# Performance work log

Hardware: AMD Instinct MI355X
Metric: run time of the kernel (lower is better)

## Reference

```python
import jax, jax.numpy as jnp
import numpy as np
import math

B, C, H, W = 16, 512, 32, 32
NUM_HEADS = 8
EPS = 1e-5

def setup_inputs() -> dict:
    key = jax.random.key(0)
    ks = jax.random.split(key, 4)
    x = jax.random.normal(ks[0], (B, C, H, W), dtype=jnp.float32)
    emb = jax.random.normal(ks[1], (B, C), dtype=jnp.float32)
    w_qkv = jax.random.normal(ks[2], (3 * C, C), dtype=jnp.float32) * (1.0 / math.sqrt(C))
    b_qkv = jnp.zeros((3 * C,), dtype=jnp.float32)
    w_proj = jax.random.normal(ks[3], (C, C), dtype=jnp.float32) * (1.0 / math.sqrt(C))
    b_proj = jnp.zeros((C,), dtype=jnp.float32)
    return {"x": x, "emb": emb, "w_qkv": w_qkv, "b_qkv": b_qkv, "w_proj": w_proj, "b_proj": b_proj}


def reference(x, emb, w_qkv, b_qkv, w_proj, b_proj):
    b, c = x.shape[0], x.shape[1]
    spatial = x.shape[2:]
    xf = x.reshape(b, c, -1)                      # [b, c, T]
    # LayerNorm over channel dim (dim=1), no affine
    mu = jnp.mean(xf, axis=1, keepdims=True)
    var = jnp.var(xf, axis=1, keepdims=True)
    xn = (xf - mu) / jnp.sqrt(var + EPS)
    # 1x1 conv = channel GEMM: [3c,c] x [b,c,T] -> [b,3c,T]
    qkv = jnp.einsum('oc,bct->bot', w_qkv, xn) + b_qkv[None, :, None]
    T = qkv.shape[-1]
    qkv = qkv.reshape(b * NUM_HEADS, -1, T)       # [b*h, 3*hd, T]
    ch = qkv.shape[1] // 3
    q, k, v = jnp.split(qkv, 3, axis=1)
    scale = 1.0 / math.sqrt(math.sqrt(ch))
    w = jnp.einsum('bct,bcs->bts', q * scale, k * scale)  # [b*h, T, T]
    w = jax.nn.softmax(w.astype(jnp.float32), axis=-1).astype(qkv.dtype)
    h = jnp.einsum('bts,bcs->bct', w, v)          # [b*h, hd, T]
    h = h.reshape(b, -1, T)                        # [b, c, T]
    h = jnp.einsum('oc,bct->bot', w_proj, h) + b_proj[None, :, None]
    return (xf + h).reshape(b, c, *spatial)
```

## Files before the change

kernel.cpp:

```cpp
#include <hip/hip_runtime.h>


#define TSZ 1024
#define CCH 512
#define NBATCH 16

typedef __attribute__((ext_vector_type(8))) short short8;
typedef __attribute__((ext_vector_type(4))) float f32x4;

__device__ inline short f2bf(float f) {
  unsigned u = __builtin_bit_cast(unsigned, f);
  u += 0x7fff + ((u >> 16) & 1);
  return (short)(u >> 16);
}

__device__ inline void gl16(const void* g, void* l) {
  __builtin_amdgcn_global_load_lds((const __attribute__((address_space(1))) void*)g,
                                   (__attribute__((address_space(3))) void*)l,
                                   16, 0, 0);
}

__global__ __launch_bounds__(256) void k_cvt(const float* __restrict__ wq,
                                             const float* __restrict__ wp,
                                             short* __restrict__ wqb,
                                             short* __restrict__ wpb) {
  int i = blockIdx.x * 256 + threadIdx.x;
  const int nq = 1536 * 512;
  if (i < nq) wqb[i] = f2bf(wq[i]);
  int j = i - nq;
  if (j >= 0 && j < 512 * 512) wpb[j] = f2bf(wp[j]);
}

__global__ __launch_bounds__(256) void k_ln(const float* __restrict__ x,
                                            short* __restrict__ xnT) {
  const int b = blockIdx.x;
  const int t0 = blockIdx.y * 64;
  const int tid = threadIdx.x;
  const int tt = tid & 63, cg = tid >> 6;

  __shared__ float red[2][4][64];
  __shared__ float mu_s[64], rs_s[64];
  __shared__ float xt[64][65];

  const float* xb = x + (long)b * CCH * TSZ;

  float s = 0.f, s2 = 0.f;
  for (int c = cg * 128; c < cg * 128 + 128; ++c) {
    float v = xb[(long)c * TSZ + t0 + tt];
    s += v; s2 += v * v;
  }
  red[0][cg][tt] = s; red[1][cg][tt] = s2;
  __syncthreads();
  if (tid < 64) {
    float ss = red[0][0][tid] + red[0][1][tid] + red[0][2][tid] + red[0][3][tid];
    float qq = red[1][0][tid] + red[1][1][tid] + red[1][2][tid] + red[1][3][tid];
    float mu = ss * (1.f / 512.f);
    float var = qq * (1.f / 512.f) - mu * mu;
    mu_s[tid] = mu;
    rs_s[tid] = rsqrtf(var + 1e-5f);
  }
  __syncthreads();

  for (int c0 = 0; c0 < CCH; c0 += 64) {
    for (int i = tid; i < 64 * 64; i += 256) {
      int ci = i >> 6, t2 = i & 63;
      xt[ci][t2] = xb[(long)(c0 + ci) * TSZ + t0 + t2];
    }
    __syncthreads();
    for (int i = tid; i < 64 * 64; i += 256) {
      int cc = i & 63, t2 = i >> 6;
      float v = (xt[cc][t2] - mu_s[t2]) * rs_s[t2];
      xnT[((long)b * TSZ + t0 + t2) * CCH + c0 + cc] = f2bf(v);
    }
    __syncthreads();
  }
}

__device__ inline int qkmap(int n) {
  if (n < 512) return (n >> 6) * 192 + (n & 63);
  int j = n - 512;
  return (j >> 6) * 192 + 64 + (j & 63);
}
__device__ inline int vmap(int m) {
  return (m >> 6) * 192 + 128 + (m & 63);
}

template <int MODE>
__global__ __launch_bounds__(256) void k_gemm(const short* __restrict__ Ab,
                                              const short* __restrict__ Bb,
                                              void* __restrict__ outb,
                                              const float* __restrict__ bias,
                                              const float* __restrict__ resid) {
  const int b = blockIdx.z;
  const int m0 = blockIdx.x * 128, n0 = blockIdx.y * 128;
  const int tid = threadIdx.x;
  const int lane = tid & 63, wv = tid >> 6;
  const int wm = wv >> 1, wn = wv & 1;
  const int l15 = lane & 15, lg = lane >> 4;

  const short* A = Ab + (MODE == 0 ? (long)b * TSZ * CCH : 0);
  const short* Bm = Bb + (MODE == 0 ? 0 : (long)b * TSZ * CCH);

  __shared__ __attribute__((aligned(16))) short sA[128 * 32];
  __shared__ __attribute__((aligned(16))) short sB[128 * 32];

  f32x4 acc[4][4];
#pragma unroll
  for (int i = 0; i < 4; ++i)
#pragma unroll
    for (int j = 0; j < 4; ++j) acc[i][j] = (f32x4){0.f, 0.f, 0.f, 0.f};

  long a_src[2], b_src[2];
#pragma unroll
  for (int q = 0; q < 2; ++q) {
    int idx = wv * 128 + q * 64 + lane;
    int row = idx >> 2, kc = (idx & 3) * 8;
    int am = m0 + row;
    int ar = (MODE == 1) ? vmap(am) : am;
    a_src[q] = (long)ar * CCH + kc;
    int bn = n0 + row;
    int br = (MODE == 0) ? qkmap(bn) : bn;
    b_src[q] = (long)br * CCH + kc;
  }

  for (int k0 = 0; k0 < CCH; k0 += 32) {
#pragma unroll
    for (int q = 0; q < 2; ++q) {
      gl16(A + a_src[q] + k0, sA + (wv * 128 + q * 64) * 8);
      gl16(Bm + b_src[q] + k0, sB + (wv * 128 + q * 64) * 8);
    }
    __syncthreads();
    short8 af[4], bfr[4];
#pragma unroll
    for (int i = 0; i < 4; ++i)
      af[i] = *(const short8*)(sA + ((wm * 64 + i * 16 + l15) * 32 + lg * 8));
#pragma unroll
    for (int j = 0; j < 4; ++j)
      bfr[j] = *(const short8*)(sB + ((wn * 64 + j * 16 + l15) * 32 + lg * 8));
#pragma unroll
    for (int i = 0; i < 4; ++i)
#pragma unroll
      for (int j = 0; j < 4; ++j)
        acc[i][j] = __builtin_amdgcn_mfma_f32_16x16x32_bf16(af[i], bfr[j], acc[i][j], 0, 0, 0);
    __syncthreads();
  }

#pragma unroll
  for (int i = 0; i < 4; ++i)
#pragma unroll
    for (int j = 0; j < 4; ++j)
#pragma unroll
      for (int r = 0; r < 4; ++r) {
        int mi = m0 + wm * 64 + i * 16 + lg * 4 + r;
        int ni = n0 + wn * 64 + j * 16 + l15;
        float val = acc[i][j][r];
        long o = (long)mi * TSZ + ni;
        if (MODE == 0) {
          val += bias[qkmap(ni)];
          if (ni < 512) val *= 0.18033688011112042f;
          ((short*)outb)[(long)b * TSZ * TSZ + o] = f2bf(val);
        } else if (MODE == 1) {
          val += bias[vmap(mi)];
          ((short*)outb)[(long)b * CCH * TSZ + o] = f2bf(val);
        } else {
          val += bias[mi] + resid[(long)b * CCH * TSZ + o];
          ((float*)outb)[(long)b * CCH * TSZ + o] = val;
        }
      }
}

__global__ __launch_bounds__(256) void k_attn(const short* __restrict__ qk,
                                              const short* __restrict__ vbuf,
                                              short* __restrict__ hb) {
  const int bh = blockIdx.y;
  const int b = bh >> 3, h = bh & 7;
  const int t0 = blockIdx.x * 128;
  const int tid = threadIdx.x;
  const int lane = tid & 63, w = tid >> 6;
  const int l15 = lane & 15, lg = lane >> 4;

  __shared__ __attribute__((aligned(16))) short kt[64 * 64];
  __shared__ __attribute__((aligned(16))) short vt[64 * 64];
  __shared__ __attribute__((aligned(16))) short pt[4][32 * 64];

  const short* qkb = qk + (long)b * TSZ * 1024;
  const short* vb = vbuf + (long)b * CCH * TSZ;

  short8 aq[2][2];
  {
    const short* qb = qkb + (long)(t0 + w * 32) * 1024 + h * 64;
#pragma unroll
    for (int i = 0; i < 2; ++i)
#pragma unroll
      for (int kk = 0; kk < 2; ++kk)
        aq[i][kk] = *(const short8*)(qb + (long)(i * 16 + l15) * 1024 + kk * 32 + lg * 8);
  }

  f32x4 of[2][4];
  float lp[2][4];
#pragma unroll
  for (int i = 0; i < 2; ++i) {
#pragma unroll
    for (int nf = 0; nf < 4; ++nf) of[i][nf] = (f32x4){0.f, 0.f, 0.f, 0.f};
#pragma unroll
    for (int r = 0; r < 4; ++r) lp[i][r] = 0.f;
  }

  int srow[2], scoff[2];
#pragma unroll
  for (int q = 0; q < 2; ++q) {
    int idx = w * 128 + q * 64 + lane;
    int row = idx >> 3;
    int byo = ((idx & 7) * 16) ^ ((row & 7) << 4);
    srow[q] = row;
    scoff[q] = byo >> 1;
  }

  for (int s0 = 0; s0 < TSZ; s0 += 64) {
#pragma unroll
    for (int q = 0; q < 2; ++q) {
      gl16(qkb + (long)(s0 + srow[q]) * 1024 + 512 + h * 64 + scoff[q],
           kt + (w * 128 + q * 64) * 8);
      gl16(vb + ((long)(h * 64 + srow[q])) * TSZ + s0 + scoff[q],
           vt + (w * 128 + q * 64) * 8);
    }
    __syncthreads();

    f32x4 sf[2][4];
#pragma unroll
    for (int i = 0; i < 2; ++i)
#pragma unroll
      for (int nf = 0; nf < 4; ++nf) sf[i][nf] = (f32x4){0.f, 0.f, 0.f, 0.f};
#pragma unroll
    for (int kk = 0; kk < 2; ++kk)
#pragma unroll
      for (int nf = 0; nf < 4; ++nf) {
        int scol = nf * 16 + l15;
        int byo = ((scol * 64 + kk * 32 + lg * 8) * 2) ^ ((scol & 7) << 4);
        short8 bk = *(const short8*)((const char*)kt + byo);
#pragma unroll
        for (int i = 0; i < 2; ++i)
          sf[i][nf] = __builtin_amdgcn_mfma_f32_16x16x32_bf16(aq[i][kk], bk, sf[i][nf], 0, 0, 0);
      }

#pragma unroll
    for (int i = 0; i < 2; ++i) {
      float p[4][4];
#pragma unroll
      for (int nf = 0; nf < 4; ++nf)
#pragma unroll
        for (int r = 0; r < 4; ++r)
          p[nf][r] = exp2f(sf[i][nf][r]);
#pragma unroll
      for (int r = 0; r < 4; ++r)
        lp[i][r] += (p[0][r] + p[1][r]) + (p[2][r] + p[3][r]);
#pragma unroll
      for (int r = 0; r < 4; ++r) {
        int tl = i * 16 + lg * 4 + r;
        int rowb = tl * 128;
        int swz = (tl & 7) << 4;
#pragma unroll
        for (int np = 0; np < 2; ++np) {
          unsigned pk;
          asm("v_cvt_pk_bf16_f32 %0, %1, %2" : "=v"(pk)
              : "v"(p[2 * np][r]), "v"(p[2 * np + 1][r]));
          int c0 = (2 * np) * 16 + l15;
          int b0 = (rowb + c0 * 2) ^ swz;
          int b1 = (rowb + (c0 + 16) * 2) ^ swz;
          *(short*)((char*)pt[w] + b0) = (short)(pk & 0xffff);
          *(short*)((char*)pt[w] + b1) = (short)(pk >> 16);
        }
      }
    }

#pragma unroll
    for (int kk = 0; kk < 2; ++kk) {
      short8 ap[2];
#pragma unroll
      for (int i = 0; i < 2; ++i) {
        int tl = i * 16 + l15;
        int byo = ((tl * 64 + kk * 32 + lg * 8) * 2) ^ ((tl & 7) << 4);
        ap[i] = *(const short8*)((const char*)pt[w] + byo);
      }
#pragma unroll
      for (int nf = 0; nf < 4; ++nf) {
        int cc = nf * 16 + l15;
        int byo = ((cc * 64 + kk * 32 + lg * 8) * 2) ^ ((cc & 7) << 4);
        short8 bv = *(const short8*)((const char*)vt + byo);
#pragma unroll
        for (int i = 0; i < 2; ++i)
          of[i][nf] = __builtin_amdgcn_mfma_f32_16x16x32_bf16(ap[i], bv, of[i][nf], 0, 0, 0);
      }
    }
    __syncthreads();
  }

  float linv[2][4];
#pragma unroll
  for (int i = 0; i < 2; ++i)
#pragma unroll
    for (int r = 0; r < 4; ++r) {
      float ls = lp[i][r];
#pragma unroll
      for (int d = 1; d < 16; d <<= 1) ls += __shfl_xor(ls, d);
      linv[i][r] = 1.0f / ls;
    }

#pragma unroll
  for (int i = 0; i < 2; ++i)
#pragma unroll
    for (int nf = 0; nf < 4; ++nf)
#pragma unroll
      for (int r = 0; r < 4; ++r) {
        int t = t0 + w * 32 + i * 16 + lg * 4 + r;
        int c = h * 64 + nf * 16 + l15;
        hb[((long)b * TSZ + t) * CCH + c] = f2bf(of[i][nf][r] * linv[i][r]);
      }
}

extern "C" void kernel_launch(void* const* d_in, const int* in_sizes, int n_in,
                              void* d_out, int out_size, void* d_ws, size_t ws_size,
                              hipStream_t stream) {
  const float* x = (const float*)d_in[0];
  const float* wq = (const float*)d_in[2];
  const float* bq = (const float*)d_in[3];
  const float* wp = (const float*)d_in[4];
  const float* bp = (const float*)d_in[5];

  char* ws = (char*)d_ws;
  short* wqb = (short*)ws;  ws += (long)1536 * 512 * 2;
  short* wpb = (short*)ws;  ws += (long)512 * 512 * 2;
  short* xnT = (short*)ws;  ws += (long)NBATCH * TSZ * CCH * 2;
  short* qkb = (short*)ws;  ws += (long)NBATCH * TSZ * 1024 * 2;
  short* vb  = (short*)ws;  ws += (long)NBATCH * CCH * TSZ * 2;
  short* hbuf = xnT;

  k_cvt<<<4096, 256, 0, stream>>>(wq, wp, wqb, wpb);
  k_ln<<<dim3(NBATCH, 16), 256, 0, stream>>>(x, xnT);
  k_gemm<0><<<dim3(8, 8, NBATCH), 256, 0, stream>>>(xnT, wqb, qkb, bq, nullptr);
  k_gemm<1><<<dim3(4, 8, NBATCH), 256, 0, stream>>>(wqb, xnT, vb, bq, nullptr);
  k_attn<<<dim3(8, 128), 256, 0, stream>>>(qkb, vb, hbuf);
  k_gemm<2><<<dim3(4, 8, NBATCH), 256, 0, stream>>>(wpb, hbuf, d_out, bp, x);
}
```

Baseline: 271.6 us.

## Double-buffer K/V tiles, transpose S MFMA, and remap attention blocks per XCD

The K and V LDS tiles become double-buffered, so the next tile's global-to-LDS load is issued before computing on the current one and the load latency overlaps with MFMA work. The QK^T MFMA swaps its operands so each lane holds one query row's scores. This lets the P tile be written as packed 32-bit stores and reduces the row-sum to two cross-lane shuffles. Blocks are also remapped so all blocks of a head land on the same XCD for L2 locality, at the cost of twice the K/V LDS footprint.

```diff
diff --git a/kernel.cpp b/kernel.cpp
--- a/kernel.cpp
+++ b/kernel.cpp
@@ -172,15 +172,17 @@
 __global__ __launch_bounds__(256) void k_attn(const short* __restrict__ qk,
                                               const short* __restrict__ vbuf,
                                               short* __restrict__ hb) {
-  const int bh = blockIdx.y;
+  const int wgid = blockIdx.y * gridDim.x + blockIdx.x;
+  const int xcd = wgid & 7, kb = wgid >> 3;
+  const int bh = xcd * 16 + (kb & 15);
+  const int t0 = (kb >> 4) * 128;
   const int b = bh >> 3, h = bh & 7;
-  const int t0 = blockIdx.x * 128;
   const int tid = threadIdx.x;
   const int lane = tid & 63, w = tid >> 6;
   const int l15 = lane & 15, lg = lane >> 4;
 
-  __shared__ __attribute__((aligned(16))) short kt[64 * 64];
-  __shared__ __attribute__((aligned(16))) short vt[64 * 64];
+  __shared__ __attribute__((aligned(16))) short kt[2][64 * 64];
+  __shared__ __attribute__((aligned(16))) short vt[2][64 * 64];
   __shared__ __attribute__((aligned(16))) short pt[4][32 * 64];
 
   const short* qkb = qk + (long)b * TSZ * 1024;
@@ -190,21 +192,18 @@
   {
     const short* qb = qkb + (long)(t0 + w * 32) * 1024 + h * 64;
 #pragma unroll
-    for (int i = 0; i < 2; ++i)
+    for (int jt = 0; jt < 2; ++jt)
 #pragma unroll
       for (int kk = 0; kk < 2; ++kk)
-        aq[i][kk] = *(const short8*)(qb + (long)(i * 16 + l15) * 1024 + kk * 32 + lg * 8);
+        aq[jt][kk] = *(const short8*)(qb + (long)(jt * 16 + l15) * 1024 + kk * 32 + lg * 8);
   }
 
   f32x4 of[2][4];
-  float lp[2][4];
-#pragma unroll
-  for (int i = 0; i < 2; ++i) {
+  float lp[2] = {0.f, 0.f};
+#pragma unroll
+  for (int i = 0; i < 2; ++i)
 #pragma unroll
     for (int nf = 0; nf < 4; ++nf) of[i][nf] = (f32x4){0.f, 0.f, 0.f, 0.f};
-#pragma unroll
-    for (int r = 0; r < 4; ++r) lp[i][r] = 0.f;
-  }
 
   int srow[2], scoff[2];
 #pragma unroll
@@ -216,61 +215,64 @@
     scoff[q] = byo >> 1;
   }
 
+#define STAGE(buf, s0s)                                                        \
+  {                                                                            \
+    _Pragma("unroll") for (int q = 0; q < 2; ++q) {                            \
+      gl16(qkb + (long)((s0s) + srow[q]) * 1024 + 512 + h * 64 + scoff[q],     \
+           kt[buf] + (w * 128 + q * 64) * 8);                                  \
+      gl16(vb + ((long)(h * 64 + srow[q])) * TSZ + (s0s) + scoff[q],           \
+           vt[buf] + (w * 128 + q * 64) * 8);                                  \
+    }                                                                          \
+  }
+
+  STAGE(0, 0);
+  __syncthreads();
+
   for (int s0 = 0; s0 < TSZ; s0 += 64) {
-#pragma unroll
-    for (int q = 0; q < 2; ++q) {
-      gl16(qkb + (long)(s0 + srow[q]) * 1024 + 512 + h * 64 + scoff[q],
-           kt + (w * 128 + q * 64) * 8);
-      gl16(vb + ((long)(h * 64 + srow[q])) * TSZ + s0 + scoff[q],
-           vt + (w * 128 + q * 64) * 8);
-    }
-    __syncthreads();
+    const int cur = (s0 >> 6) & 1;
+    if (s0 + 64 < TSZ) STAGE(cur ^ 1, s0 + 64);
 
     f32x4 sf[2][4];
 #pragma unroll
-    for (int i = 0; i < 2; ++i)
-#pragma unroll
-      for (int nf = 0; nf < 4; ++nf) sf[i][nf] = (f32x4){0.f, 0.f, 0.f, 0.f};
+    for (int jt = 0; jt < 2; ++jt)
+#pragma unroll
+      for (int ms = 0; ms < 4; ++ms) sf[jt][ms] = (f32x4){0.f, 0.f, 0.f, 0.f};
 #pragma unroll
     for (int kk = 0; kk < 2; ++kk)
 #pragma unroll
-      for (int nf = 0; nf < 4; ++nf) {
-        int scol = nf * 16 + l15;
-        int byo = ((scol * 64 + kk * 32 + lg * 8) * 2) ^ ((scol & 7) << 4);
-        short8 bk = *(const short8*)((const char*)kt + byo);
-#pragma unroll
-        for (int i = 0; i < 2; ++i)
-          sf[i][nf] = __builtin_amdgcn_mfma_f32_16x16x32_bf16(aq[i][kk], bk, sf[i][nf], 0, 0, 0);
-      }
-
-#pragma unroll
-    for (int i = 0; i < 2; ++i) {
+      for (int ms = 0; ms < 4; ++ms) {
+        int srw = ms * 16 + l15;
+        int byo = ((srw * 64 + kk * 32 + lg * 8) * 2) ^ ((srw & 7) << 4);
+        short8 ka = *(const short8*)((const char*)kt[cur] + byo);
+#pragma unroll
+        for (int jt = 0; jt < 2; ++jt)
+          sf[jt][ms] = __builtin_amdgcn_mfma_f32_16x16x32_bf16(ka, aq[jt][kk], sf[jt][ms], 0, 0, 0);
+      }
+
+#pragma unroll
+    for (int jt = 0; jt < 2; ++jt) {
       float p[4][4];
 #pragma unroll
-      for (int nf = 0; nf < 4; ++nf)
+      for (int ms = 0; ms < 4; ++ms)
 #pragma unroll
         for (int r = 0; r < 4; ++r)
-          p[nf][r] = exp2f(sf[i][nf][r]);
-#pragma unroll
-      for (int r = 0; r < 4; ++r)
-        lp[i][r] += (p[0][r] + p[1][r]) + (p[2][r] + p[3][r]);
-#pragma unroll
-      for (int r = 0; r < 4; ++r) {
-        int tl = i * 16 + lg * 4 + r;
-        int rowb = tl * 128;
-        int swz = (tl & 7) << 4;
-#pragma unroll
-        for (int np = 0; np < 2; ++np) {
+          p[ms][r] = exp2f(sf[jt][ms][r]);
+#pragma unroll
+      for (int ms = 0; ms < 4; ++ms)
+        lp[jt] += (p[ms][0] + p[ms][1]) + (p[ms][2] + p[ms][3]);
+      const int tl = jt * 16 + l15;
+      const int rowb = tl * 128;
+      const int swz = (tl & 7) << 4;
+#pragma unroll
+      for (int ms = 0; ms < 4; ++ms)
+#pragma unroll
+        for (int u = 0; u < 2; ++u) {
           unsigned pk;
           asm("v_cvt_pk_bf16_f32 %0, %1, %2" : "=v"(pk)
-              : "v"(p[2 * np][r]), "v"(p[2 * np + 1][r]));
-          int c0 = (2 * np) * 16 + l15;
-          int b0 = (rowb + c0 * 2) ^ swz;
-          int b1 = (rowb + (c0 + 16) * 2) ^ swz;
-          *(short*)((char*)pt[w] + b0) = (short)(pk & 0xffff);
-          *(short*)((char*)pt[w] + b1) = (short)(pk >> 16);
+              : "v"(p[ms][2 * u]), "v"(p[ms][2 * u + 1]));
+          int sl = ms * 16 + lg * 4 + 2 * u;
+          *(unsigned*)((char*)pt[w] + ((rowb + sl * 2) ^ swz)) = pk;
         }
-      }
     }
 
 #pragma unroll
@@ -286,7 +288,7 @@
       for (int nf = 0; nf < 4; ++nf) {
         int cc = nf * 16 + l15;
         int byo = ((cc * 64 + kk * 32 + lg * 8) * 2) ^ ((cc & 7) << 4);
-        short8 bv = *(const short8*)((const char*)vt + byo);
+        short8 bv = *(const short8*)((const char*)vt[cur] + byo);
 #pragma unroll
         for (int i = 0; i < 2; ++i)
           of[i][nf] = __builtin_amdgcn_mfma_f32_16x16x32_bf16(ap[i], bv, of[i][nf], 0, 0, 0);
@@ -297,14 +299,14 @@
 
   float linv[2][4];
 #pragma unroll
-  for (int i = 0; i < 2; ++i)
-#pragma unroll
-    for (int r = 0; r < 4; ++r) {
-      float ls = lp[i][r];
-#pragma unroll
-      for (int d = 1; d < 16; d <<= 1) ls += __shfl_xor(ls, d);
-      linv[i][r] = 1.0f / ls;
-    }
+  for (int i = 0; i < 2; ++i) {
+    float ls = lp[i];
+    ls += __shfl_xor(ls, 16);
+    ls += __shfl_xor(ls, 32);
+#pragma unroll
+    for (int r = 0; r < 4; ++r)
+      linv[i][r] = 1.0f / __shfl(ls, lg * 4 + r);
+  }
 
 #pragma unroll
   for (int i = 0; i < 2; ++i)
```

New measurement: 256.4 us. 1.06x faster.
